# Optimization experiments

Hardware: AMD Instinct MI355X
Metric: run time of the kernel (lower is better)

## Reference

```python
import jax, jax.numpy as jnp
import numpy as np
from jax import lax

B, N, D, S, K = 8, 4096, 61, 1024, 32
MLP = (64, 64, 128)
WN = (3, 8, 8, 16)  # WeightNet: 3 -> 8 -> 8 -> 16
EPS = 1e-5


def _gather(p, idx):
    # p: [B, N, C], idx: [B, ...] -> [B, ..., C]
    return jax.vmap(lambda pb, ib: pb[ib])(p, idx)


def _fps(xyz, npoint, key):
    # farthest point sampling, xyz: [B, N, 3] -> idx [B, npoint]
    b, n, _ = xyz.shape
    start = jax.random.randint(key, (b,), 0, n)
    def step(carry, _):
        dmin, far = carry
        centroid = jnp.take_along_axis(xyz, far[:, None, None], axis=1)  # [B,1,3]
        d = jnp.sum((xyz - centroid) ** 2, -1)                            # [B,N]
        dmin = jnp.minimum(dmin, d)
        return (dmin, jnp.argmax(dmin, -1)), far
    _, idxs = lax.scan(step, (jnp.full((b, n), 1e10, xyz.dtype), start), None, length=npoint)
    return idxs.T  # [B, npoint]


def _sqdist(a, b):
    # a: [B,S,3], b: [B,N,3] -> [B,S,N]
    return (jnp.sum(a ** 2, -1)[:, :, None] + jnp.sum(b ** 2, -1)[:, None, :]
            - 2.0 * jnp.einsum('bsc,bnc->bsn', a, b))


def _bn_relu(x, g, be):
    # channels-last BN (training-mode batch stats, biased var) + ReLU
    axes = tuple(range(x.ndim - 1))
    m = x.mean(axes, keepdims=True)
    v = x.var(axes, keepdims=True)
    return jax.nn.relu(g * (x - m) * lax.rsqrt(v + EPS) + be)


def _forward(xyz, points, mlp_p, wn_p, lin_w, lin_b, bnl_g, bnl_b):
    xyz_t = xyz.transpose(0, 2, 1)    # [B,N,3]
    pts = points.transpose(0, 2, 1)   # [B,N,D]
    xyz_sg = lax.stop_gradient(xyz_t)  # index computations carry no grads (as in torch)
    fps_idx = _fps(xyz_sg, S, jax.random.key(42))  # [B,S]
    new_xyz = _gather(xyz_t, fps_idx)              # [B,S,3]
    idx = lax.top_k(-_sqdist(lax.stop_gradient(new_xyz), xyz_sg), K)[1]  # [B,S,K]
    g_norm = _gather(xyz_t, idx) - new_xyz[:, :, None, :]                # [B,S,K,3]
    feat = jnp.concatenate([g_norm, _gather(pts, idx)], -1)              # [B,S,K,3+D]
    for w, b, g, be in mlp_p:
        feat = _bn_relu(jnp.einsum('bskc,oc->bsko', feat, w) + b, g, be)
    wts = g_norm
    for w, b, g, be in wn_p:
        wts = _bn_relu(jnp.einsum('bskc,oc->bsko', wts, w) + b, g, be)   # [B,S,K,16]
    # [B,S,C,K] @ [B,S,K,16] -> [B,S,C,16] -> [B,S,C*16] (C-major flatten, as torch .view)
    agg = jnp.einsum('bskc,bskw->bscw', feat, wts).reshape(B, S, -1)
    out = agg @ lin_w.T + lin_b                                          # [B,S,128]
    m = out.mean((0, 1), keepdims=True)  # BatchNorm1d over batch and spatial
    v = out.var((0, 1), keepdims=True)
    out = jax.nn.relu(bnl_g * (out - m) * lax.rsqrt(v + EPS) + bnl_b)
    return new_xyz.transpose(0, 2, 1), out.transpose(0, 2, 1)  # [B,3,S], [B,128,S]


def setup_inputs() -> dict:
    key = jax.random.key(0)
    ks = iter(jax.random.split(key, 64))
    inp = {"xyz": jax.random.normal(next(ks), (B, 3, N), jnp.float32),
           "points": jax.random.normal(next(ks), (B, D, N), jnp.float32)}
    mlp_in = (3 + D,) + MLP[:-1]
    for i, (ci, co) in enumerate(zip(mlp_in, MLP)):
        inp[f"mlp_w{i}"] = jax.random.normal(next(ks), (co, ci), jnp.float32) / np.float32(np.sqrt(ci))
        inp[f"mlp_b{i}"] = jnp.zeros((co,), jnp.float32)
        inp[f"mlp_g{i}"] = jnp.ones((co,), jnp.float32)
        inp[f"mlp_be{i}"] = jnp.zeros((co,), jnp.float32)
    for i, (ci, co) in enumerate(zip(WN[:-1], WN[1:])):
        inp[f"wn_w{i}"] = jax.random.normal(next(ks), (co, ci), jnp.float32) / np.float32(np.sqrt(ci))
        inp[f"wn_b{i}"] = jnp.zeros((co,), jnp.float32)
        inp[f"wn_g{i}"] = jnp.ones((co,), jnp.float32)
        inp[f"wn_be{i}"] = jnp.zeros((co,), jnp.float32)
    fin = 16 * MLP[-1]
    inp["lin_w"] = jax.random.normal(next(ks), (MLP[-1], fin), jnp.float32) / np.float32(np.sqrt(fin))
    inp["lin_b"] = jnp.zeros((MLP[-1],), jnp.float32)
    inp["bnl_g"] = jnp.ones((MLP[-1],), jnp.float32)
    inp["bnl_b"] = jnp.zeros((MLP[-1],), jnp.float32)
    return inp


def reference(xyz, points, mlp_w0, mlp_b0, mlp_g0, mlp_be0, mlp_w1, mlp_b1, mlp_g1, mlp_be1, mlp_w2, mlp_b2, mlp_g2, mlp_be2, wn_w0, wn_b0, wn_g0, wn_be0, wn_w1, wn_b1, wn_g1, wn_be1, wn_w2, wn_b2, wn_g2, wn_be2, lin_w, lin_b, bnl_g, bnl_b):
    mlp_p = [(mlp_w0, mlp_b0, mlp_g0, mlp_be0),
             (mlp_w1, mlp_b1, mlp_g1, mlp_be1),
             (mlp_w2, mlp_b2, mlp_g2, mlp_be2)]
    wn_p = [(wn_w0, wn_b0, wn_g0, wn_be0),
            (wn_w1, wn_b1, wn_g1, wn_be1),
            (wn_w2, wn_b2, wn_g2, wn_be2)]
    return _forward(xyz, points, mlp_p, wn_p, lin_w, lin_b, bnl_g, bnl_b)
```

## Files before the change

kernel.cpp:

```cpp
#include <hip/hip_runtime.h>
#include <cstdint>
#include <cstddef>


constexpr int B_ = 8, N_ = 4096, D_ = 61, S_ = 1024, K_ = 32;
constexpr int P_ = B_ * S_ * K_;
constexpr int BS_ = B_ * S_;

constexpr size_t OFF_STATS  = 0;
constexpr size_t OFF_NEWXYZ = 8192;
constexpr size_t OFF_KNN    = 106496;
constexpr size_t OFF_PT     = 1155072;
constexpr size_t OFF_Y01    = 9543680;
constexpr size_t OFF_Y2     = 76652544;
constexpr size_t OFF_W01    = 210870272;
constexpr size_t OFF_W2B    = 219258880;
constexpr size_t OFF_OUTPRE = OFF_W01;

static inline uint32_t rotl32(uint32_t x, int r){ return (x << r) | (x >> (32 - r)); }
static void tf2x32(uint32_t k0, uint32_t k1, uint32_t x0, uint32_t x1,
                   uint32_t* o0, uint32_t* o1){
  uint32_t ks[3] = {k0, k1, k0 ^ k1 ^ 0x1BD11BDAu};
  x0 += ks[0]; x1 += ks[1];
  const int RA[4] = {13,15,26,6}, RB[4] = {17,29,16,24};
// ... 5 lines not shown
  *o0 = x0; *o1 = x1;
}
struct StartIdx { int v[8]; };
static StartIdx compute_starts(){
  uint32_t ka, kb;
  tf2x32(0u, 42u, 0u, 1u, &ka, &kb);
  StartIdx s;
  for (int i = 0; i < 8; ++i){
    uint32_t b1, b2;
    tf2x32(ka, kb, 0u, (uint32_t)i, &b1, &b2);
    s.v[i] = (int)((b1 ^ b2) & 4095u);
  }
  return s;
}

template<int C>
__device__ __forceinline__ float dpp_max_f32_step(float x){
  int t = __builtin_amdgcn_update_dpp(0, (int)__float_as_uint(x), C, 0xf, 0xf, true);
  return fmaxf(x, __uint_as_float((unsigned)t));
}
__device__ __forceinline__ float dpp_wave_max_f32(float x){
  x = dpp_max_f32_step<0x111>(x);
  x = dpp_max_f32_step<0x112>(x);
  x = dpp_max_f32_step<0x114>(x);
  x = dpp_max_f32_step<0x118>(x);
  x = dpp_max_f32_step<0x142>(x);
  x = dpp_max_f32_step<0x143>(x);
  return __uint_as_float((unsigned)__builtin_amdgcn_readlane((int)__float_as_uint(x), 63));
}
template<int C>
__device__ __forceinline__ unsigned dpp_min_u32_step(unsigned x){
  int t = __builtin_amdgcn_update_dpp(-1, (int)x, C, 0xf, 0xf, false);
  unsigned u = (unsigned)t;
  return u < x ? u : x;
}
__device__ __forceinline__ unsigned dpp_wave_min_u32(unsigned x){
  x = dpp_min_u32_step<0x111>(x);
  x = dpp_min_u32_step<0x112>(x);
  x = dpp_min_u32_step<0x114>(x);
  x = dpp_min_u32_step<0x118>(x);
  x = dpp_min_u32_step<0x142>(x);
  x = dpp_min_u32_step<0x143>(x);
  return (unsigned)__builtin_amdgcn_readlane((int)x, 63);
}
template<int C>
__device__ __forceinline__ unsigned long long dpp_min_u64_step(unsigned long long k){
  unsigned lo = (unsigned)k, hi = (unsigned)(k >> 32);
  unsigned olo = (unsigned)__builtin_amdgcn_update_dpp(-1, (int)lo, C, 0xf, 0xf, false);
  unsigned ohi = (unsigned)__builtin_amdgcn_update_dpp(-1, (int)hi, C, 0xf, 0xf, false);
  unsigned long long o = ((unsigned long long)ohi << 32) | olo;
  return o < k ? o : k;
}
__device__ __forceinline__ unsigned long long dpp_wave_min_u64(unsigned long long k){
  k = dpp_min_u64_step<0x111>(k);
  k = dpp_min_u64_step<0x112>(k);
  k = dpp_min_u64_step<0x114>(k);
  k = dpp_min_u64_step<0x118>(k);
  k = dpp_min_u64_step<0x142>(k);
  k = dpp_min_u64_step<0x143>(k);
  unsigned lo = (unsigned)__builtin_amdgcn_readlane((int)(unsigned)k, 63);
  unsigned hi = (unsigned)__builtin_amdgcn_readlane((int)(unsigned)(k >> 32), 63);
  return ((unsigned long long)hi << 32) | lo;
}
template<int C>
__device__ __forceinline__ float dpp_add_step(float x){
  int t = __builtin_amdgcn_update_dpp(0, (int)__float_as_uint(x), C, 0xf, 0xf, true);
  return x + __uint_as_float((unsigned)t);
}
__device__ __forceinline__ float dpp_row_sum16(float x){
  x = dpp_add_step<0x111>(x);
  x = dpp_add_step<0x112>(x);
  x = dpp_add_step<0x114>(x);
  x = dpp_add_step<0x118>(x);
  return x;
}
__device__ __forceinline__ unsigned ordf(float f){
  unsigned u = __float_as_uint(f);
  return u ^ (unsigned)(((int)u >> 31) | 0x80000000);
}
__device__ __forceinline__ void atomAddD(double* p, double v){
  __hip_atomic_fetch_add(p, v, __ATOMIC_RELAXED, __HIP_MEMORY_SCOPE_AGENT);
}

#define REP16(M) M(0) M(1) M(2) M(3) M(4) M(5) M(6) M(7) \
                 M(8) M(9) M(10) M(11) M(12) M(13) M(14) M(15)

__global__ __launch_bounds__(256, 1) void fps_tr_kernel(const float* __restrict__ xyz,
                                                        const float* __restrict__ pts,
                                                        StartIdx st,
                                                        float* __restrict__ new_xyz,
                                                        float* __restrict__ out_xyz,
                                                        float* __restrict__ pT){
  __shared__ float4 pts4[N_];
  __shared__ unsigned short win[S_];
  __shared__ unsigned long long slotK[2][4];
  __shared__ float4 slotC[2][4];
  const int tid = threadIdx.x;

  if (blockIdx.x >= 8){
    float* tile = (float*)pts4;
    const int tt = blockIdx.x - 8;
    const int b = tt >> 6, n0 = (tt & 63) * 64;
    for (int e = tid; e < 61*64; e += 256){
      int d = e >> 6, c = e & 63;
      tile[d*65 + c] = pts[((size_t)b*61 + d)*N_ + n0 + c];
    }
    __syncthreads();
    for (int e = tid; e < 4096; e += 256){
      int r = e >> 6, d = e & 63;
      pT[((size_t)b*N_ + n0 + r)*64 + d] = (d < 61) ? tile[d*65 + r] : 0.f;
    }
    return;
  }

  const int b = blockIdx.x;
  const int lane = tid & 63, wv = tid >> 6;
  const float* xb = xyz + (size_t)b*3*N_;

#define LOADP(i) \
  float px##i = xb[tid + 256*(i)]; \
  float py##i = xb[N_ + tid + 256*(i)]; \
  float pz##i = xb[2*N_ + tid + 256*(i)]; \
  float dm##i = 1e10f; \
  pts4[tid + 256*(i)] = make_float4(px##i, py##i, pz##i, 0.f);
  REP16(LOADP)
#undef LOADP
  __syncthreads();

  int cur = st.v[b];
  float4 c4 = pts4[cur];
  float cx = c4.x, cy = c4.y, cz = c4.z;

  int par = 0;
  for (int s = 0; s < S_; ++s){
    if (tid == 0) win[s] = (unsigned short)cur;
#define UPD(i) { \
      float dx = __fsub_rn(px##i, cx), dy = __fsub_rn(py##i, cy), dz = __fsub_rn(pz##i, cz); \
      float d  = __fadd_rn(__fadd_rn(__fmul_rn(dx,dx), __fmul_rn(dy,dy)), __fmul_rn(dz,dz)); \
      dm##i = fminf(dm##i, d); }
    REP16(UPD)
#undef UPD
    float a0 = fmaxf(dm0, dm1),  a1 = fmaxf(dm2, dm3);
    float a2 = fmaxf(dm4, dm5),  a3 = fmaxf(dm6, dm7);
    float a4 = fmaxf(dm8, dm9),  a5 = fmaxf(dm10, dm11);
    float a6 = fmaxf(dm12, dm13),a7 = fmaxf(dm14, dm15);
    float b0 = fmaxf(a0, a1), b1 = fmaxf(a2, a3), b2 = fmaxf(a4, a5), b3 = fmaxf(a6, a7);
    float lmax = fmaxf(fmaxf(b0, b1), fmaxf(b2, b3));
    const float wmax = dpp_wave_max_f32(lmax);
#define CANDI(i) unsigned c##i = (dm##i == wmax) ? (unsigned)(tid | ((i) << 8)) : 0xFFFFFFFFu;
    REP16(CANDI)
#undef CANDI
    unsigned d0 = c0  < c1  ? c0  : c1,  d1 = c2  < c3  ? c2  : c3;
    unsigned d2 = c4  < c5  ? c4  : c5,  d3 = c6  < c7  ? c6  : c7;
    unsigned d4 = c8  < c9  ? c8  : c9,  d5 = c10 < c11 ? c10 : c11;
    unsigned d6 = c12 < c13 ? c12 : c13, d7 = c14 < c15 ? c14 : c15;
    unsigned e0 = d0 < d1 ? d0 : d1, e1 = d2 < d3 ? d2 : d3;
    unsigned e2 = d4 < d5 ? d4 : d5, e3 = d6 < d7 ? d6 : d7;
    unsigned f0 = e0 < e1 ? e0 : e1, f1 = e2 < e3 ? e2 : e3;
    unsigned cand = f0 < f1 ? f0 : f1;
    const unsigned widx = dpp_wave_min_u32(cand);
    if (tid == (int)(widx & 255u)){
      const int sl = (int)(widx >> 8);
      float sx = px0, sy = py0, sz = pz0;
#define SEL(i) if (sl == (i)){ sx = px##i; sy = py##i; sz = pz##i; }
      SEL(1) SEL(2) SEL(3) SEL(4) SEL(5) SEL(6) SEL(7) SEL(8)
      SEL(9) SEL(10) SEL(11) SEL(12) SEL(13) SEL(14) SEL(15)
#undef SEL
      slotK[par][wv] = ((unsigned long long)__float_as_uint(wmax) << 32)
                     | (unsigned long long)(unsigned)(~widx);
      slotC[par][wv] = make_float4(sx, sy, sz, 0.f);
    }
    __syncthreads();
    unsigned long long k0 = slotK[par][0], k1 = slotK[par][1],
                       k2 = slotK[par][2], k3 = slotK[par][3];
    float4 q0 = slotC[par][0], q1 = slotC[par][1],
           q2 = slotC[par][2], q3 = slotC[par][3];
    unsigned long long m0 = k0; float4 g0 = q0;
    if (k1 > m0){ m0 = k1; g0 = q1; }
    unsigned long long m1 = k2; float4 g1 = q2;
    if (k3 > m1){ m1 = k3; g1 = q3; }
    if (m1 > m0){ m0 = m1; g0 = g1; }
    cur = (int)(~(unsigned)m0) & (N_ - 1);
    cx = g0.x; cy = g0.y; cz = g0.z;
    par ^= 1;
  }
  __syncthreads();
  for (int s2 = tid; s2 < S_; s2 += 256){
    float4 p = pts4[win[s2]];
    new_xyz[((size_t)b*S_ + s2)*3 + 0] = p.x;
    new_xyz[((size_t)b*S_ + s2)*3 + 1] = p.y;
    new_xyz[((size_t)b*S_ + s2)*3 + 2] = p.z;
    out_xyz[(size_t)b*3*S_ + s2]        = p.x;
    out_xyz[(size_t)b*3*S_ + S_ + s2]   = p.y;
    out_xyz[(size_t)b*3*S_ + 2*S_ + s2] = p.z;
  }
}
#undef REP16

__global__ __launch_bounds__(256) void knn_kernel(const float* __restrict__ xyz,
                                                  const float* __restrict__ nxyz,
                                                  int* __restrict__ knn_idx){
  __shared__ float dist[4][4096];
  const int wv = threadIdx.x >> 6, lane = threadIdx.x & 63;
  const int q = blockIdx.x*4 + wv;
  const int b = q >> 10;
  const float* xb = xyz + (size_t)b*3*N_;
  const float ax = nxyz[(size_t)q*3], ay = nxyz[(size_t)q*3+1], az = nxyz[(size_t)q*3+2];
  const float sa = __fadd_rn(__fadd_rn(__fmul_rn(ax,ax), __fmul_rn(ay,ay)), __fmul_rn(az,az));
  float* dw = dist[wv];
  unsigned long long kk = ~0ull;
  for (int i = 0; i < 64; ++i){
    int n = i*64 + lane;
    float x = xb[n], y = xb[N_+n], z = xb[2*N_+n];
    float sb  = __fadd_rn(__fadd_rn(__fmul_rn(x,x), __fmul_rn(y,y)), __fmul_rn(z,z));
    float dot = __fadd_rn(__fadd_rn(__fmul_rn(ax,x), __fmul_rn(ay,y)), __fmul_rn(az,z));
    float d   = __fsub_rn(__fadd_rn(sa, sb), __fmul_rn(2.f, dot));
    dw[i*64 + ((lane + i) & 63)] = d;
    unsigned long long key = ((unsigned long long)ordf(d) << 32) | (unsigned)n;
    if (key < kk) kk = key;
  }
  __syncthreads();
  int myout = 0;
  for (int r = 0; r < 32; ++r){
    unsigned long long g = dpp_wave_min_u64(kk);
    const int gn = (int)(g & 0xFFFFFFFFull);
    if (lane == r) myout = gn;
    const int col = gn & 63, row = gn >> 6;
    const int a = lane*64 + ((col + lane) & 63);
    float v = dw[a];
    if (lane == row){ v = 3.4e38f; dw[a] = 3.4e38f; }
    unsigned long long nk = ((unsigned long long)ordf(v) << 32)
                          | (unsigned)(lane*64 + col);
    nk = dpp_wave_min_u64(nk);
    if (lane == col) kk = nk;
  }
  if (lane < 32) knn_idx[(size_t)q*32 + lane] = myout;
}

__device__ __forceinline__ void bn_coeff(const double* st, const float* g, const float* be,
                                         int c, double cnt, float* sc, float* sh){
  double mean = st[c*2] / cnt;
  double var  = st[c*2+1] / cnt - mean*mean;
  double scale = (double)g[c] / sqrt(var + 1e-5);
  *sc = (float)scale; *sh = (float)((double)be[c] - mean*scale);
}

#define STATS64(ACC_EXPR, ST, CH_OFF)                                          \
  {                                                                            \
    _Pragma("unroll")                                                          \
    for (int o = 0; o < 64; ++o){                                              \
      float v_ = (ACC_EXPR);                                                   \
      float s1_ = dpp_row_sum16(v_);                                           \
      float q1_ = dpp_row_sum16(v_*v_);                                        \
      if ((threadIdx.x & 15) == 15){                                           \
        int rid_ = threadIdx.x >> 4;                                           \
        redS[rid_][o] = s1_; redQ[rid_][o] = q1_;                              \
      }                                                                        \
    }                                                                          \
    __syncthreads();                                                           \
    if (threadIdx.x < 64){                                                     \
      float s_ = 0.f;                                                          \
      _Pragma("unroll")                                                        \
      for (int r_ = 0; r_ < 16; ++r_) s_ += redS[r_][threadIdx.x];             \
      atomAddD(&(ST)[((CH_OFF) + threadIdx.x)*2], (double)s_);                 \
    } else if (threadIdx.x < 128){                                             \
      int o_ = threadIdx.x - 64;                                               \
      float s_ = 0.f;                                                          \
      _Pragma("unroll")                                                        \
      for (int r_ = 0; r_ < 16; ++r_) s_ += redQ[r_][o_];                      \
      atomAddD(&(ST)[((CH_OFF) + o_)*2 + 1], (double)s_);                      \
    }                                                                          \
  }

__global__ __launch_bounds__(256, 2) void m0_kernel(const float* __restrict__ pT,
                                                    const float* __restrict__ xyz,
                                                    const float* __restrict__ nxyz,
                                                    const int* __restrict__ knn_idx,
                                                    const float* __restrict__ w,
                                                    const float* __restrict__ bias,
                                                    float* __restrict__ y,
                                                    double* __restrict__ stout){
  __shared__ float Wt[4096]; __shared__ float bb[64];
  __shared__ float redS[16][65], redQ[16][65];
  for (int t = threadIdx.x; t < 4096; t += 256){ int o = t >> 6, c = t & 63; Wt[c*64+o] = w[o*64+c]; }
  if (threadIdx.x < 64) bb[threadIdx.x] = bias[threadIdx.x];
  __syncthreads();
  const int p = blockIdx.x*256 + threadIdx.x;
  const int b = p >> 15, s = (p & 32767) >> 5;
  const int n = knn_idx[p];
  float in[64];
  {
    const float* xb = xyz + (size_t)b*3*N_;
    const int q = (b << 10) + s;
    in[0] = xb[n]       - nxyz[(size_t)q*3];
    in[1] = xb[N_+n]    - nxyz[(size_t)q*3+1];
    in[2] = xb[2*N_+n]  - nxyz[(size_t)q*3+2];
    const float* pr = pT + ((size_t)b*N_ + n)*64;
#pragma unroll
    for (int d = 0; d < 60; d += 4){
      float4 v = *reinterpret_cast<const float4*>(&pr[d]);
      in[3+d] = v.x; in[4+d] = v.y; in[5+d] = v.z; in[6+d] = v.w;
    }
    in[63] = pr[60];
  }
  float acc[64];
#pragma unroll
  for (int o = 0; o < 64; ++o) acc[o] = bb[o];
#pragma unroll
  for (int c = 0; c < 64; ++c){
    float x = in[c];
#pragma unroll
    for (int o = 0; o < 64; o += 4){
      float4 w4 = *reinterpret_cast<const float4*>(&Wt[c*64+o]);
      acc[o]   += x*w4.x; acc[o+1] += x*w4.y; acc[o+2] += x*w4.z; acc[o+3] += x*w4.w;
    }
  }
#pragma unroll
  for (int o = 0; o < 64; ++o) y[(size_t)o*P_ + p] = acc[o];
  STATS64(acc[o], stout, 0)
}

__global__ __launch_bounds__(256, 2) void m1_kernel(float* __restrict__ y,
                                                    const float* __restrict__ w,
                                                    const float* __restrict__ bias,
                                                    const double* __restrict__ stin,
                                                    const float* __restrict__ g,
                                                    const float* __restrict__ be,
                                                    double* __restrict__ stout){
  __shared__ float Wt[4096]; __shared__ float bb[64], sc[64], sh[64];
  __shared__ float redS[16][65], redQ[16][65];
  for (int t = threadIdx.x; t < 4096; t += 256){ int o = t >> 6, c = t & 63; Wt[c*64+o] = w[o*64+c]; }
  if (threadIdx.x < 64){
    bn_coeff(stin, g, be, threadIdx.x, (double)P_, &sc[threadIdx.x], &sh[threadIdx.x]);
    bb[threadIdx.x] = bias[threadIdx.x];
  }
  __syncthreads();
  const int p = blockIdx.x*256 + threadIdx.x;
  float in[64];
#pragma unroll
  for (int c = 0; c < 64; ++c){
    float x = y[(size_t)c*P_ + p];
    in[c] = fmaxf(0.f, fmaf(x, sc[c], sh[c]));
  }
  float acc[64];
#pragma unroll
  for (int o = 0; o < 64; ++o) acc[o] = bb[o];
#pragma unroll
  for (int c = 0; c < 64; ++c){
    float x = in[c];
#pragma unroll
    for (int o = 0; o < 64; o += 4){
      float4 w4 = *reinterpret_cast<const float4*>(&Wt[c*64+o]);
      acc[o]   += x*w4.x; acc[o+1] += x*w4.y; acc[o+2] += x*w4.z; acc[o+3] += x*w4.w;
    }
  }
#pragma unroll
  for (int o = 0; o < 64; ++o) y[(size_t)o*P_ + p] = acc[o];
  STATS64(acc[o], stout, 0)
}

__global__ __launch_bounds__(256, 2) void m2_kernel(const float* __restrict__ y1,
                                                    float* __restrict__ y2,
                                                    const float* __restrict__ w,
                                                    const float* __restrict__ bias,
                                                    const double* __restrict__ stin,
                                                    const float* __restrict__ g,
                                                    const float* __restrict__ be,
                                                    double* __restrict__ stout){
  __shared__ float Wt[4096]; __shared__ float bb[64], sc[64], sh[64];
  __shared__ float redS[16][65], redQ[16][65];
  const int half = blockIdx.y;
  for (int t = threadIdx.x; t < 4096; t += 256){
    int o = t >> 6, c = t & 63;
    Wt[c*64+o] = w[(size_t)(half*64+o)*64 + c];
  }
  if (threadIdx.x < 64){
    bn_coeff(stin, g, be, threadIdx.x, (double)P_, &sc[threadIdx.x], &sh[threadIdx.x]);
    bb[threadIdx.x] = bias[half*64 + threadIdx.x];
  }
  __syncthreads();
  const int p = blockIdx.x*256 + threadIdx.x;
  float in[64];
#pragma unroll
  for (int c = 0; c < 64; ++c){
    float x = y1[(size_t)c*P_ + p];
    in[c] = fmaxf(0.f, fmaf(x, sc[c], sh[c]));
  }
  float acc[64];
#pragma unroll
  for (int o = 0; o < 64; ++o) acc[o] = bb[o];
#pragma unroll
  for (int c = 0; c < 64; ++c){
    float x = in[c];
#pragma unroll
    for (int o = 0; o < 64; o += 4){
      float4 w4 = *reinterpret_cast<const float4*>(&Wt[c*64+o]);
      acc[o]   += x*w4.x; acc[o+1] += x*w4.y; acc[o+2] += x*w4.z; acc[o+3] += x*w4.w;
    }
  }
#pragma unroll
  for (int o = 0; o < 64; ++o) y2[(size_t)(half*64+o)*P_ + p] = acc[o];
  STATS64(acc[o], stout, half*64)
}

__global__ __launch_bounds__(256) void w0_kernel(const float* __restrict__ xyz,
                                                 const float* __restrict__ nxyz,
                                                 const int* __restrict__ knn_idx,
                                                 const float* __restrict__ w,
                                                 const float* __restrict__ bias,
                                                 float* __restrict__ wb,
                                                 double* __restrict__ stout){
  __shared__ float Wl[24], bb[8];
  __shared__ float redS[16][9], redQ[16][9];
  if (threadIdx.x < 24) Wl[threadIdx.x] = w[threadIdx.x];
  if (threadIdx.x < 8)  bb[threadIdx.x] = bias[threadIdx.x];
  __syncthreads();
  const int p = blockIdx.x*256 + threadIdx.x;
  const int b = p >> 15, s = (p & 32767) >> 5;
  const int n = knn_idx[p];
  const float* xb = xyz + (size_t)b*3*N_;
  const int q = (b << 10) + s;
  float gx = xb[n]      - nxyz[(size_t)q*3];
  float gy = xb[N_+n]   - nxyz[(size_t)q*3+1];
  float gz = xb[2*N_+n] - nxyz[(size_t)q*3+2];
  float a_[8];
#pragma unroll
  for (int o = 0; o < 8; ++o){
    a_[o] = bb[o] + gx*Wl[o*3] + gy*Wl[o*3+1] + gz*Wl[o*3+2];
    wb[(size_t)o*P_ + p] = a_[o];
  }
#pragma unroll
  for (int o = 0; o < 8; ++o){
    float s1 = dpp_row_sum16(a_[o]);
    float q1 = dpp_row_sum16(a_[o]*a_[o]);
    if ((threadIdx.x & 15) == 15){ int rid = threadIdx.x >> 4; redS[rid][o] = s1; redQ[rid][o] = q1; }
  }
  __syncthreads();
  if (threadIdx.x < 8){
    float s_ = 0.f;
#pragma unroll
    for (int r = 0; r < 16; ++r) s_ += redS[r][threadIdx.x];
    atomAddD(&stout[threadIdx.x*2], (double)s_);
  } else if (threadIdx.x < 16){
    int o = threadIdx.x - 8;
    float s_ = 0.f;
#pragma unroll
    for (int r = 0; r < 16; ++r) s_ += redQ[r][o];
    atomAddD(&stout[o*2+1], (double)s_);
  }
}

__global__ __launch_bounds__(256) void w1_kernel(float* __restrict__ wb,
                                                 const float* __restrict__ w,
                                                 const float* __restrict__ bias,
                                                 const double* __restrict__ stin,
                                                 const float* __restrict__ g,
                                                 const float* __restrict__ be,
                                                 double* __restrict__ stout){
  __shared__ float Wl[64], bb[8], sc[8], sh[8];
  __shared__ float redS[16][9], redQ[16][9];
  if (threadIdx.x < 64) Wl[threadIdx.x] = w[threadIdx.x];
  if (threadIdx.x < 8){
    bn_coeff(stin, g, be, threadIdx.x, (double)P_, &sc[threadIdx.x], &sh[threadIdx.x]);
    bb[threadIdx.x] = bias[threadIdx.x];
  }
  __syncthreads();
  const int p = blockIdx.x*256 + threadIdx.x;
  float in[8];
#pragma unroll
  for (int c = 0; c < 8; ++c){
    float x = wb[(size_t)c*P_ + p];
    in[c] = fmaxf(0.f, fmaf(x, sc[c], sh[c]));
  }
  float acc[8];
#pragma unroll
  for (int o = 0; o < 8; ++o){
    float a = bb[o];
#pragma unroll
    for (int c = 0; c < 8; ++c) a += in[c]*Wl[o*8+c];
    acc[o] = a;
  }
#pragma unroll
  for (int o = 0; o < 8; ++o) wb[(size_t)o*P_ + p] = acc[o];
#pragma unroll
  for (int o = 0; o < 8; ++o){
    float s1 = dpp_row_sum16(acc[o]);
    float q1 = dpp_row_sum16(acc[o]*acc[o]);
    if ((threadIdx.x & 15) == 15){ int rid = threadIdx.x >> 4; redS[rid][o] = s1; redQ[rid][o] = q1; }
  }
  __syncthreads();
  if (threadIdx.x < 8){
    float s_ = 0.f;
#pragma unroll
    for (int r = 0; r < 16; ++r) s_ += redS[r][threadIdx.x];
    atomAddD(&stout[threadIdx.x*2], (double)s_);
  } else if (threadIdx.x < 16){
    int o = threadIdx.x - 8;
    float s_ = 0.f;
#pragma unroll
    for (int r = 0; r < 16; ++r) s_ += redQ[r][o];
    atomAddD(&stout[o*2+1], (double)s_);
  }
}

__global__ __launch_bounds__(256) void w2_kernel(const float* __restrict__ wb,
                                                 float* __restrict__ wb2,
                                                 const float* __restrict__ w,
                                                 const float* __restrict__ bias,
                                                 const double* __restrict__ stin,
                                                 const float* __restrict__ g,
                                                 const float* __restrict__ be,
                                                 double* __restrict__ stout){
  __shared__ float Wl[128], bb[16], sc[8], sh[8];
  __shared__ float redS[16][17], redQ[16][17];
  if (threadIdx.x < 128) Wl[threadIdx.x] = w[threadIdx.x];
  if (threadIdx.x < 8)
    bn_coeff(stin, g, be, threadIdx.x, (double)P_, &sc[threadIdx.x], &sh[threadIdx.x]);
  if (threadIdx.x < 16) bb[threadIdx.x] = bias[threadIdx.x];
  __syncthreads();
  const int p = blockIdx.x*256 + threadIdx.x;
  float in[8];
#pragma unroll
  for (int c = 0; c < 8; ++c){
    float x = wb[(size_t)c*P_ + p];
    in[c] = fmaxf(0.f, fmaf(x, sc[c], sh[c]));
  }
  float acc[16];
#pragma unroll
  for (int o = 0; o < 16; ++o){
    float a = bb[o];
#pragma unroll
    for (int c = 0; c < 8; ++c) a += in[c]*Wl[o*8+c];
    acc[o] = a;
    wb2[(size_t)o*P_ + p] = a;
  }
#pragma unroll
  for (int o = 0; o < 16; ++o){
    float s1 = dpp_row_sum16(acc[o]);
    float q1 = dpp_row_sum16(acc[o]*acc[o]);
    if ((threadIdx.x & 15) == 15){ int rid = threadIdx.x >> 4; redS[rid][o] = s1; redQ[rid][o] = q1; }
  }
  __syncthreads();
  if (threadIdx.x < 16){
    float s_ = 0.f;
#pragma unroll
    for (int r = 0; r < 16; ++r) s_ += redS[r][threadIdx.x];
    atomAddD(&stout[threadIdx.x*2], (double)s_);
  } else if (threadIdx.x < 32){
    int o = threadIdx.x - 16;
    float s_ = 0.f;
#pragma unroll
    for (int r = 0; r < 16; ++r) s_ += redQ[r][o];
    atomAddD(&stout[o*2+1], (double)s_);
  }
}

__global__ __launch_bounds__(256) void agg_kernel(const float* __restrict__ y2,
                                                  const float* __restrict__ wb2,
                                                  const double* __restrict__ st2,
                                                  const float* __restrict__ g2,
                                                  const float* __restrict__ be2,
                                                  const double* __restrict__ stw,
                                                  const float* __restrict__ gw,
                                                  const float* __restrict__ bew,
                                                  float* __restrict__ agg){
  __shared__ float f[32*132];
  __shared__ float wt[32*16];
  __shared__ float sc2[128], sh2[128], scw[16], shw[16];
  const int t = threadIdx.x;
  if (t < 128) bn_coeff(st2, g2, be2, t, (double)P_, &sc2[t], &sh2[t]);
  if (t < 16)  bn_coeff(stw, gw, bew, t, (double)P_, &scw[t], &shw[t]);
  __syncthreads();
  const int bs = blockIdx.x;
  const size_t p0 = (size_t)bs * 32;
  for (int e = t; e < 4096; e += 256){
    int c = e >> 5, k = e & 31;
    float x = y2[(size_t)c*P_ + p0 + k];
    f[k*132 + c] = fmaxf(0.f, fmaf(x, sc2[c], sh2[c]));
  }
  for (int e = t; e < 512; e += 256){
    int w = e >> 5, k = e & 31;
    float x = wb2[(size_t)w*P_ + p0 + k];
    wt[k*16 + w] = fmaxf(0.f, fmaf(x, scw[w], shw[w]));
  }
  __syncthreads();
  const int c = t >> 1, wp = (t & 1) * 8;
  float a0=0,a1=0,a2=0,a3=0,a4=0,a5=0,a6=0,a7=0;
#pragma unroll
  for (int k = 0; k < 32; ++k){
    float fv = f[k*132 + c];
    float4 u = *reinterpret_cast<const float4*>(&wt[k*16 + wp]);
    float4 v = *reinterpret_cast<const float4*>(&wt[k*16 + wp + 4]);
    a0 += fv*u.x; a1 += fv*u.y; a2 += fv*u.z; a3 += fv*u.w;
    a4 += fv*v.x; a5 += fv*v.y; a6 += fv*v.z; a7 += fv*v.w;
  }
  float* dst = agg + (size_t)bs*2048 + c*16 + wp;
  *reinterpret_cast<float4*>(dst)     = make_float4(a0,a1,a2,a3);
  *reinterpret_cast<float4*>(dst + 4) = make_float4(a4,a5,a6,a7);
}

__global__ __launch_bounds__(256) void lin_kernel(const float* __restrict__ agg,
                                                  const float* __restrict__ lw,
                                                  const float* __restrict__ lb,
                                                  float* __restrict__ outp){
  __shared__ float A[32*33];
  __shared__ float Wl[32*128];
  __shared__ float lbs[128];
  const int t = threadIdx.x;
  const int r0 = blockIdx.x * 32;
  if (t < 128) lbs[t] = lb[t];
  const int c_lane = t & 31, rg = t >> 5;
  float acc[4][4];
#pragma unroll
  for (int i = 0; i < 4; ++i)
#pragma unroll
    for (int j = 0; j < 4; ++j) acc[i][j] = 0.f;

  for (int kk0 = 0; kk0 < 2048; kk0 += 32){
    __syncthreads();
    {
      int r = t >> 3, kq = (t & 7) * 4;
      float4 v = *reinterpret_cast<const float4*>(&agg[(size_t)(r0 + r)*2048 + kk0 + kq]);
      A[r*33 + kq]   = v.x; A[r*33 + kq+1] = v.y; A[r*33 + kq+2] = v.z; A[r*33 + kq+3] = v.w;
    }
    {
#pragma unroll
      for (int u = 0; u < 4; ++u){
        int fid = t + 256*u;
        int o = fid >> 3, kq = (fid & 7) * 4;
        float4 v = *reinterpret_cast<const float4*>(&lw[(size_t)o*2048 + kk0 + kq]);
        Wl[(kq  )*128 + o] = v.x; Wl[(kq+1)*128 + o] = v.y;
        Wl[(kq+2)*128 + o] = v.z; Wl[(kq+3)*128 + o] = v.w;
      }
    }
    __syncthreads();
#pragma unroll 8
// ... 19 lines not shown

__global__ __launch_bounds__(128) void statsF_kernel(const float* __restrict__ outp,
                                                     double* __restrict__ st){
  const int c = threadIdx.x;
  const int r0 = blockIdx.x * 128;
  double s = 0.0, q = 0.0;
  for (int r = 0; r < 128; ++r){
    double v = outp[(size_t)(r0 + r)*128 + c];
    s += v; q += v*v;
  }
  atomAddD(&st[c*2], s); atomAddD(&st[c*2+1], q);
}

__global__ __launch_bounds__(256) void final_kernel(const float* __restrict__ outp,
                                                    const double* __restrict__ st,
                                                    const float* __restrict__ g,
                                                    const float* __restrict__ be,
                                                    float* __restrict__ out){
  __shared__ float sc[128], sh[128];
  __shared__ float tile[64][129];
  const int t = threadIdx.x;
  if (t < 128) bn_coeff(st, g, be, t, (double)BS_, &sc[t], &sh[t]);
  const int bs0 = blockIdx.x * 64;
  const int b = bs0 >> 10, s0 = bs0 & 1023;
#pragma unroll
  for (int e = t; e < 8192; e += 256){
    int r = e >> 7, c = e & 127;
    tile[r][c] = outp[(size_t)(bs0 + r)*128 + c];
  }
  __syncthreads();
#pragma unroll
  for (int e = t; e < 8192; e += 256){
    int o = e >> 6, si = e & 63;
    float x = tile[si][o];
    out[(size_t)b*131072 + (size_t)o*1024 + s0 + si] = fmaxf(0.f, fmaf(x, sc[o], sh[o]));
  }
}

extern "C" void kernel_launch(void* const* d_in, const int* in_sizes, int n_in,
                              void* d_out, int out_size, void* d_ws, size_t ws_size,
                              hipStream_t stream){
  (void)in_sizes; (void)n_in; (void)out_size; (void)ws_size;
  const float* xyz    = (const float*)d_in[0];
  const float* points = (const float*)d_in[1];
  const float* mw0 = (const float*)d_in[2],  *mb0 = (const float*)d_in[3],
             * mg0 = (const float*)d_in[4],  *me0 = (const float*)d_in[5];
  const float* mw1 = (const float*)d_in[6],  *mb1 = (const float*)d_in[7],
             * mg1 = (const float*)d_in[8],  *me1 = (const float*)d_in[9];
  const float* mw2 = (const float*)d_in[10], *mb2 = (const float*)d_in[11],
             * mg2 = (const float*)d_in[12], *me2 = (const float*)d_in[13];
  const float* ww0 = (const float*)d_in[14], *wb0 = (const float*)d_in[15],
             * wg0 = (const float*)d_in[16], *we0 = (const float*)d_in[17];
  const float* ww1 = (const float*)d_in[18], *wb1 = (const float*)d_in[19],
             * wg1 = (const float*)d_in[20], *we1 = (const float*)d_in[21];
  const float* ww2 = (const float*)d_in[22], *wb2_ = (const float*)d_in[23],
             * wg2 = (const float*)d_in[24], *we2 = (const float*)d_in[25];
  const float* lw  = (const float*)d_in[26], *lb  = (const float*)d_in[27];
  const float* fg  = (const float*)d_in[28], *fb  = (const float*)d_in[29];

  char* ws = (char*)d_ws;
  double* ST0 = (double*)(ws + OFF_STATS);
  double* ST1 = (double*)(ws + OFF_STATS + 1024);
  double* ST2 = (double*)(ws + OFF_STATS + 2048);
  double* SW0 = (double*)(ws + OFF_STATS + 4096);
  double* SW1 = (double*)(ws + OFF_STATS + 4224);
  double* SW2 = (double*)(ws + OFF_STATS + 4352);
  double* STF = (double*)(ws + OFF_STATS + 4608);
  float* nxyz   = (float*)(ws + OFF_NEWXYZ);
  int*   knnidx = (int*)(ws + OFF_KNN);
  float* pT     = (float*)(ws + OFF_PT);
  float* y01    = (float*)(ws + OFF_Y01);
  float* y2     = (float*)(ws + OFF_Y2);
  float* w01    = (float*)(ws + OFF_W01);
  float* w2b    = (float*)(ws + OFF_W2B);
  float* aggbuf = (float*)(ws + OFF_Y01);
  float* outpre = (float*)(ws + OFF_OUTPRE);

  float* out_xyz  = (float*)d_out;
  float* out_feat = (float*)d_out + (size_t)B_*3*S_;

  hipMemsetAsync(ws + OFF_STATS, 0, 8192, stream);

  StartIdx st = compute_starts();
  fps_tr_kernel<<<dim3(8 + B_*64), dim3(256), 0, stream>>>(xyz, points, st, nxyz, out_xyz, pT);

  knn_kernel<<<dim3(BS_/4), dim3(256), 0, stream>>>(xyz, nxyz, knnidx);

  m0_kernel<<<dim3(P_/256), dim3(256), 0, stream>>>(pT, xyz, nxyz, knnidx, mw0, mb0, y01, ST0);
  m1_kernel<<<dim3(P_/256), dim3(256), 0, stream>>>(y01, mw1, mb1, ST0, mg0, me0, ST1);
  m2_kernel<<<dim3(P_/256, 2), dim3(256), 0, stream>>>(y01, y2, mw2, mb2, ST1, mg1, me1, ST2);

  w0_kernel<<<dim3(P_/256), dim3(256), 0, stream>>>(xyz, nxyz, knnidx, ww0, wb0, w01, SW0);
  w1_kernel<<<dim3(P_/256), dim3(256), 0, stream>>>(w01, ww1, wb1, SW0, wg0, we0, SW1);
  w2_kernel<<<dim3(P_/256), dim3(256), 0, stream>>>(w01, w2b, ww2, wb2_, SW1, wg1, we1, SW2);

  agg_kernel<<<dim3(BS_), dim3(256), 0, stream>>>(y2, w2b, ST2, mg2, me2, SW2, wg2, we2, aggbuf);
  lin_kernel<<<dim3(BS_/32), dim3(256), 0, stream>>>(aggbuf, lw, lb, outpre);
  statsF_kernel<<<dim3(BS_/128), dim3(128), 0, stream>>>(outpre, STF);
  final_kernel<<<dim3(BS_/64), dim3(256), 0, stream>>>(outpre, STF, fg, fb, out_feat);
}
```

Measured before the change: 1.772 ms.

## Fuse WeightNet layers into MLP kernels and widen FPS block to 512 threads

The three WeightNet kernels (w0/w1/w2) are folded into the corresponding MLP layer kernels, so the gathered xyz offsets and per-point work share one launch and one index gather. This removes three launches and the separate xyz re-gather. FPS now runs with 512 threads per batch, 8 points per thread instead of 16, and a cross-wave reduction over 8 waves. It also skips the unused distance update on the final iteration. The trade-off is more registers and shared memory in the fused MLP kernels, and an extra wave in the per-iteration FPS barrier reduction.

```diff
diff --git a/kernel.cpp b/kernel.cpp
--- a/kernel.cpp
+++ b/kernel.cpp
@@ -111,10 +111,9 @@
   __hip_atomic_fetch_add(p, v, __ATOMIC_RELAXED, __HIP_MEMORY_SCOPE_AGENT);
 }
 
-#define REP16(M) M(0) M(1) M(2) M(3) M(4) M(5) M(6) M(7) \
-                 M(8) M(9) M(10) M(11) M(12) M(13) M(14) M(15)
-
-__global__ __launch_bounds__(256, 1) void fps_tr_kernel(const float* __restrict__ xyz,
+#define REP8(M) M(0) M(1) M(2) M(3) M(4) M(5) M(6) M(7)
+
+__global__ __launch_bounds__(512, 1) void fps_tr_kernel(const float* __restrict__ xyz,
                                                         const float* __restrict__ pts,
                                                         StartIdx st,
                                                         float* __restrict__ new_xyz,
@@ -122,20 +121,20 @@
                                                         float* __restrict__ pT){
   __shared__ float4 pts4[N_];
   __shared__ unsigned short win[S_];
-  __shared__ unsigned long long slotK[2][4];
-  __shared__ float4 slotC[2][4];
+  __shared__ unsigned long long slotK[2][8];
+  __shared__ float4 slotC[2][8];
   const int tid = threadIdx.x;
 
   if (blockIdx.x >= 8){
     float* tile = (float*)pts4;
     const int tt = blockIdx.x - 8;
     const int b = tt >> 6, n0 = (tt & 63) * 64;
-    for (int e = tid; e < 61*64; e += 256){
+    for (int e = tid; e < 61*64; e += 512){
       int d = e >> 6, c = e & 63;
       tile[d*65 + c] = pts[((size_t)b*61 + d)*N_ + n0 + c];
     }
     __syncthreads();
-    for (int e = tid; e < 4096; e += 256){
+    for (int e = tid; e < 4096; e += 512){
       int r = e >> 6, d = e & 63;
       pT[((size_t)b*N_ + n0 + r)*64 + d] = (d < 61) ? tile[d*65 + r] : 0.f;
     }
@@ -147,12 +146,12 @@
   const float* xb = xyz + (size_t)b*3*N_;
 
 #define LOADP(i) \
-  float px##i = xb[tid + 256*(i)]; \
-  float py##i = xb[N_ + tid + 256*(i)]; \
-  float pz##i = xb[2*N_ + tid + 256*(i)]; \
+  float px##i = xb[tid + 512*(i)]; \
+  float py##i = xb[N_ + tid + 512*(i)]; \
+  float pz##i = xb[2*N_ + tid + 512*(i)]; \
   float dm##i = 1e10f; \
-  pts4[tid + 256*(i)] = make_float4(px##i, py##i, pz##i, 0.f);
-  REP16(LOADP)
+  pts4[tid + 512*(i)] = make_float4(px##i, py##i, pz##i, 0.f);
+  REP8(LOADP)
 #undef LOADP
   __syncthreads();
 
@@ -163,37 +162,30 @@
   int par = 0;
   for (int s = 0; s < S_; ++s){
     if (tid == 0) win[s] = (unsigned short)cur;
+    if (s == S_ - 1) break;
 #define UPD(i) { \
       float dx = __fsub_rn(px##i, cx), dy = __fsub_rn(py##i, cy), dz = __fsub_rn(pz##i, cz); \
       float d  = __fadd_rn(__fadd_rn(__fmul_rn(dx,dx), __fmul_rn(dy,dy)), __fmul_rn(dz,dz)); \
       dm##i = fminf(dm##i, d); }
-    REP16(UPD)
+    REP8(UPD)
 #undef UPD
-    float a0 = fmaxf(dm0, dm1),  a1 = fmaxf(dm2, dm3);
-    float a2 = fmaxf(dm4, dm5),  a3 = fmaxf(dm6, dm7);
-    float a4 = fmaxf(dm8, dm9),  a5 = fmaxf(dm10, dm11);
-    float a6 = fmaxf(dm12, dm13),a7 = fmaxf(dm14, dm15);
-    float b0 = fmaxf(a0, a1), b1 = fmaxf(a2, a3), b2 = fmaxf(a4, a5), b3 = fmaxf(a6, a7);
-    float lmax = fmaxf(fmaxf(b0, b1), fmaxf(b2, b3));
+    float a0 = fmaxf(dm0, dm1), a1 = fmaxf(dm2, dm3);
+    float a2 = fmaxf(dm4, dm5), a3 = fmaxf(dm6, dm7);
+    float lmax = fmaxf(fmaxf(a0, a1), fmaxf(a2, a3));
     const float wmax = dpp_wave_max_f32(lmax);
-#define CANDI(i) unsigned c##i = (dm##i == wmax) ? (unsigned)(tid | ((i) << 8)) : 0xFFFFFFFFu;
-    REP16(CANDI)
+#define CANDI(i) unsigned c##i = (dm##i == wmax) ? (unsigned)(tid | ((i) << 9)) : 0xFFFFFFFFu;
+    REP8(CANDI)
 #undef CANDI
-    unsigned d0 = c0  < c1  ? c0  : c1,  d1 = c2  < c3  ? c2  : c3;
-    unsigned d2 = c4  < c5  ? c4  : c5,  d3 = c6  < c7  ? c6  : c7;
-    unsigned d4 = c8  < c9  ? c8  : c9,  d5 = c10 < c11 ? c10 : c11;
-    unsigned d6 = c12 < c13 ? c12 : c13, d7 = c14 < c15 ? c14 : c15;
+    unsigned d0 = c0 < c1 ? c0 : c1, d1 = c2 < c3 ? c2 : c3;
+    unsigned d2 = c4 < c5 ? c4 : c5, d3 = c6 < c7 ? c6 : c7;
     unsigned e0 = d0 < d1 ? d0 : d1, e1 = d2 < d3 ? d2 : d3;
-    unsigned e2 = d4 < d5 ? d4 : d5, e3 = d6 < d7 ? d6 : d7;
-    unsigned f0 = e0 < e1 ? e0 : e1, f1 = e2 < e3 ? e2 : e3;
-    unsigned cand = f0 < f1 ? f0 : f1;
+    unsigned cand = e0 < e1 ? e0 : e1;
     const unsigned widx = dpp_wave_min_u32(cand);
-    if (tid == (int)(widx & 255u)){
-      const int sl = (int)(widx >> 8);
+    if (tid == (int)(widx & 511u)){
+      const int sl = (int)(widx >> 9);
       float sx = px0, sy = py0, sz = pz0;
 #define SEL(i) if (sl == (i)){ sx = px##i; sy = py##i; sz = pz##i; }
-      SEL(1) SEL(2) SEL(3) SEL(4) SEL(5) SEL(6) SEL(7) SEL(8)
-      SEL(9) SEL(10) SEL(11) SEL(12) SEL(13) SEL(14) SEL(15)
+      SEL(1) SEL(2) SEL(3) SEL(4) SEL(5) SEL(6) SEL(7)
 #undef SEL
       slotK[par][wv] = ((unsigned long long)__float_as_uint(wmax) << 32)
                      | (unsigned long long)(unsigned)(~widx);
@@ -201,20 +193,26 @@
     }
     __syncthreads();
     unsigned long long k0 = slotK[par][0], k1 = slotK[par][1],
-                       k2 = slotK[par][2], k3 = slotK[par][3];
+                       k2 = slotK[par][2], k3 = slotK[par][3],
+                       k4 = slotK[par][4], k5 = slotK[par][5],
+                       k6 = slotK[par][6], k7 = slotK[par][7];
     float4 q0 = slotC[par][0], q1 = slotC[par][1],
-           q2 = slotC[par][2], q3 = slotC[par][3];
-    unsigned long long m0 = k0; float4 g0 = q0;
-    if (k1 > m0){ m0 = k1; g0 = q1; }
-    unsigned long long m1 = k2; float4 g1 = q2;
-    if (k3 > m1){ m1 = k3; g1 = q3; }
+           q2 = slotC[par][2], q3 = slotC[par][3],
+           q4 = slotC[par][4], q5 = slotC[par][5],
+           q6 = slotC[par][6], q7 = slotC[par][7];
+    unsigned long long m0 = k0; float4 g0 = q0; if (k1 > m0){ m0 = k1; g0 = q1; }
+    unsigned long long m1 = k2; float4 g1 = q2; if (k3 > m1){ m1 = k3; g1 = q3; }
+    unsigned long long m2 = k4; float4 g2 = q4; if (k5 > m2){ m2 = k5; g2 = q5; }
+    unsigned long long m3 = k6; float4 g3 = q6; if (k7 > m3){ m3 = k7; g3 = q7; }
     if (m1 > m0){ m0 = m1; g0 = g1; }
+    if (m3 > m2){ m2 = m3; g2 = g3; }
+    if (m2 > m0){ m0 = m2; g0 = g2; }
     cur = (int)(~(unsigned)m0) & (N_ - 1);
     cx = g0.x; cy = g0.y; cz = g0.z;
     par ^= 1;
   }
   __syncthreads();
-  for (int s2 = tid; s2 < S_; s2 += 256){
+  for (int s2 = tid; s2 < S_; s2 += 512){
     float4 p = pts4[win[s2]];
     new_xyz[((size_t)b*S_ + s2)*3 + 0] = p.x;
     new_xyz[((size_t)b*S_ + s2)*3 + 1] = p.y;
@@ -224,7 +222,7 @@
     out_xyz[(size_t)b*3*S_ + 2*S_ + s2] = p.z;
   }
 }
-#undef REP16
+#undef REP8
 
 __global__ __launch_bounds__(256) void knn_kernel(const float* __restrict__ xyz,
                                                   const float* __restrict__ nxyz,
@@ -301,18 +299,52 @@
     }                                                                          \
   }
 
-__global__ __launch_bounds__(256, 2) void m0_kernel(const float* __restrict__ pT,
-                                                    const float* __restrict__ xyz,
-                                                    const float* __restrict__ nxyz,
-                                                    const int* __restrict__ knn_idx,
-                                                    const float* __restrict__ w,
-                                                    const float* __restrict__ bias,
-                                                    float* __restrict__ y,
-                                                    double* __restrict__ stout){
+#define STATSW(NC, VALS, ST)                                                   \
+  {                                                                            \
+    _Pragma("unroll")                                                          \
+    for (int o = 0; o < (NC); ++o){                                            \
+      float s1 = dpp_row_sum16(VALS[o]);                                       \
+      float q1 = dpp_row_sum16(VALS[o]*VALS[o]);                               \
+      if ((threadIdx.x & 15) == 15){                                           \
+        int rid = threadIdx.x >> 4;                                            \
+        redSW[rid][o] = s1; redQW[rid][o] = q1;                                \
+      }                                                                        \
+    }                                                                          \
+    __syncthreads();                                                           \
+    if (threadIdx.x < (NC)){                                                   \
+      float s_ = 0.f;                                                          \
+      _Pragma("unroll")                                                        \
+      for (int r = 0; r < 16; ++r) s_ += redSW[r][threadIdx.x];                \
+      atomAddD(&(ST)[threadIdx.x*2], (double)s_);                              \
+    } else if (threadIdx.x < 2*(NC)){                                          \
+      int o = threadIdx.x - (NC);                                              \
+      float s_ = 0.f;                                                          \
+      _Pragma("unroll")                                                        \
+      for (int r = 0; r < 16; ++r) s_ += redQW[r][o];                          \
+      atomAddD(&(ST)[o*2+1], (double)s_);                                      \
+    }                                                                          \
+  }
+
+__global__ __launch_bounds__(256, 2) void m0w0_kernel(const float* __restrict__ pT,
+                                                      const float* __restrict__ xyz,
+                                                      const float* __restrict__ nxyz,
+                                                      const int* __restrict__ knn_idx,
+                                                      const float* __restrict__ w,
+                                                      const float* __restrict__ bias,
+                                                      const float* __restrict__ ww0,
+                                                      const float* __restrict__ wb0,
+                                                      float* __restrict__ y,
+                                                      float* __restrict__ wbuf,
+                                                      double* __restrict__ stout,
+                                                      double* __restrict__ stw){
   __shared__ float Wt[4096]; __shared__ float bb[64];
+  __shared__ float Wl0[24], bb0[8];
   __shared__ float redS[16][65], redQ[16][65];
+  __shared__ float redSW[16][9], redQW[16][9];
   for (int t = threadIdx.x; t < 4096; t += 256){ int o = t >> 6, c = t & 63; Wt[c*64+o] = w[o*64+c]; }
   if (threadIdx.x < 64) bb[threadIdx.x] = bias[threadIdx.x];
+  if (threadIdx.x >= 64 && threadIdx.x < 88) Wl0[threadIdx.x-64] = ww0[threadIdx.x-64];
+  if (threadIdx.x >= 96 && threadIdx.x < 104) bb0[threadIdx.x-96] = wb0[threadIdx.x-96];
   __syncthreads();
   const int p = blockIdx.x*256 + threadIdx.x;
   const int b = p >> 15, s = (p & 32767) >> 5;
@@ -332,6 +364,12 @@
     }
     in[63] = pr[60];
   }
+  float wa[8];
+#pragma unroll
+  for (int o = 0; o < 8; ++o){
+    wa[o] = bb0[o] + in[0]*Wl0[o*3] + in[1]*Wl0[o*3+1] + in[2]*Wl0[o*3+2];
+    wbuf[(size_t)o*P_ + p] = wa[o];
+  }
   float acc[64];
 #pragma unroll
   for (int o = 0; o < 64; ++o) acc[o] = bb[o];
@@ -347,24 +385,57 @@
 #pragma unroll
   for (int o = 0; o < 64; ++o) y[(size_t)o*P_ + p] = acc[o];
   STATS64(acc[o], stout, 0)
-}
-
-__global__ __launch_bounds__(256, 2) void m1_kernel(float* __restrict__ y,
-                                                    const float* __restrict__ w,
-                                                    const float* __restrict__ bias,
-                                                    const double* __restrict__ stin,
-                                                    const float* __restrict__ g,
-                                                    const float* __restrict__ be,
-                                                    double* __restrict__ stout){
+  __syncthreads();
+  STATSW(8, wa, stw)
+}
+
+__global__ __launch_bounds__(256, 2) void m1w1_kernel(float* __restrict__ y,
+                                                      const float* __restrict__ w,
+                                                      const float* __restrict__ bias,
+                                                      const double* __restrict__ stin,
+                                                      const float* __restrict__ g,
+                                                      const float* __restrict__ be,
+                                                      float* __restrict__ wbuf,
+                                                      const float* __restrict__ ww1,
+                                                      const float* __restrict__ wb1,
+                                                      const double* __restrict__ stwin,
+                                                      const float* __restrict__ wg,
+                                                      const float* __restrict__ we,
+                                                      double* __restrict__ stout,
+                                                      double* __restrict__ stw){
   __shared__ float Wt[4096]; __shared__ float bb[64], sc[64], sh[64];
+  __shared__ float Wl[64], bbw[8], scw[8], shw[8];
   __shared__ float redS[16][65], redQ[16][65];
+  __shared__ float redSW[16][9], redQW[16][9];
   for (int t = threadIdx.x; t < 4096; t += 256){ int o = t >> 6, c = t & 63; Wt[c*64+o] = w[o*64+c]; }
   if (threadIdx.x < 64){
     bn_coeff(stin, g, be, threadIdx.x, (double)P_, &sc[threadIdx.x], &sh[threadIdx.x]);
     bb[threadIdx.x] = bias[threadIdx.x];
+  } else if (threadIdx.x < 128){
+    Wl[threadIdx.x-64] = ww1[threadIdx.x-64];
+  } else if (threadIdx.x < 136){
+    int o = threadIdx.x - 128;
+    bn_coeff(stwin, wg, we, o, (double)P_, &scw[o], &shw[o]);
+    bbw[o] = wb1[o];
   }
   __syncthreads();
   const int p = blockIdx.x*256 + threadIdx.x;
+  float win8[8];
+#pragma unroll
+  for (int c = 0; c < 8; ++c){
+    float x = wbuf[(size_t)c*P_ + p];
+    win8[c] = fmaxf(0.f, fmaf(x, scw[c], shw[c]));
+  }
+  float wacc[8];
+#pragma unroll
+  for (int o = 0; o < 8; ++o){
+    float a = bbw[o];
+#pragma unroll
+    for (int c = 0; c < 8; ++c) a += win8[c]*Wl[o*8+c];
+    wacc[o] = a;
+  }
+#pragma unroll
+  for (int o = 0; o < 8; ++o) wbuf[(size_t)o*P_ + p] = wacc[o];
   float in[64];
 #pragma unroll
   for (int c = 0; c < 64; ++c){
@@ -386,18 +457,30 @@
 #pragma unroll
   for (int o = 0; o < 64; ++o) y[(size_t)o*P_ + p] = acc[o];
   STATS64(acc[o], stout, 0)
-}
-
-__global__ __launch_bounds__(256, 2) void m2_kernel(const float* __restrict__ y1,
-                                                    float* __restrict__ y2,
-                                                    const float* __restrict__ w,
-                                                    const float* __restrict__ bias,
-                                                    const double* __restrict__ stin,
-                                                    const float* __restrict__ g,
-                                                    const float* __restrict__ be,
-                                                    double* __restrict__ stout){
+  __syncthreads();
+  STATSW(8, wacc, stw)
+}
+
+__global__ __launch_bounds__(256, 2) void m2w2_kernel(const float* __restrict__ y1,
+                                                      float* __restrict__ y2,
+                                                      const float* __restrict__ w,
+                                                      const float* __restrict__ bias,
+                                                      const double* __restrict__ stin,
+                                                      const float* __restrict__ g,
+                                                      const float* __restrict__ be,
+                                                      const float* __restrict__ wbuf,
+                                                      float* __restrict__ wbuf2,
+                                                      const float* __restrict__ ww2,
+                                                      const float* __restrict__ wb2,
+                                                      const double* __restrict__ stwin,
+                                                      const float* __restrict__ wg,
+                                                      const float* __restrict__ we,
+                                                      double* __restrict__ stout,
+                                                      double* __restrict__ stw){
   __shared__ float Wt[4096]; __shared__ float bb[64], sc[64], sh[64];
+  __shared__ float Wl[128], bbw[16], scw[8], shw[8];
   __shared__ float redS[16][65], redQ[16][65];
+  __shared__ float redSW[16][17], redQW[16][17];
   const int half = blockIdx.y;
   for (int t = threadIdx.x; t < 4096; t += 256){
     int o = t >> 6, c = t & 63;
@@ -406,9 +489,33 @@
   if (threadIdx.x < 64){
     bn_coeff(stin, g, be, threadIdx.x, (double)P_, &sc[threadIdx.x], &sh[threadIdx.x]);
     bb[threadIdx.x] = bias[half*64 + threadIdx.x];
+  } else if (threadIdx.x < 192){
+    Wl[threadIdx.x-64] = ww2[threadIdx.x-64];
+  } else if (threadIdx.x < 200){
+    int o = threadIdx.x - 192;
+    bn_coeff(stwin, wg, we, o, (double)P_, &scw[o], &shw[o]);
+  } else if (threadIdx.x < 216){
+    bbw[threadIdx.x-200] = wb2[threadIdx.x-200];
   }
   __syncthreads();
   const int p = blockIdx.x*256 + threadIdx.x;
+  float wacc[16];
+  if (half == 0){
+    float win8[8];
+#pragma unroll
+    for (int c = 0; c < 8; ++c){
+      float x = wbuf[(size_t)c*P_ + p];
+      win8[c] = fmaxf(0.f, fmaf(x, scw[c], shw[c]));
+    }
+#pragma unroll
+    for (int o = 0; o < 16; ++o){
+      float a = bbw[o];
+#pragma unroll
+      for (int c = 0; c < 8; ++c) a += win8[c]*Wl[o*8+c];
+      wacc[o] = a;
+      wbuf2[(size_t)o*P_ + p] = a;
+    }
+  }
   float in[64];
 #pragma unroll
   for (int c = 0; c < 64; ++c){
@@ -430,157 +537,9 @@
 #pragma unroll
   for (int o = 0; o < 64; ++o) y2[(size_t)(half*64+o)*P_ + p] = acc[o];
   STATS64(acc[o], stout, half*64)
-}
-
-__global__ __launch_bounds__(256) void w0_kernel(const float* __restrict__ xyz,
-                                                 const float* __restrict__ nxyz,
-                                                 const int* __restrict__ knn_idx,
-                                                 const float* __restrict__ w,
-                                                 const float* __restrict__ bias,
-                                                 float* __restrict__ wb,
-                                                 double* __restrict__ stout){
-  __shared__ float Wl[24], bb[8];
-  __shared__ float redS[16][9], redQ[16][9];
-  if (threadIdx.x < 24) Wl[threadIdx.x] = w[threadIdx.x];
-  if (threadIdx.x < 8)  bb[threadIdx.x] = bias[threadIdx.x];
-  __syncthreads();
-  const int p = blockIdx.x*256 + threadIdx.x;
-  const int b = p >> 15, s = (p & 32767) >> 5;
-  const int n = knn_idx[p];
-  const float* xb = xyz + (size_t)b*3*N_;
-  const int q = (b << 10) + s;
-  float gx = xb[n]      - nxyz[(size_t)q*3];
-  float gy = xb[N_+n]   - nxyz[(size_t)q*3+1];
-  float gz = xb[2*N_+n] - nxyz[(size_t)q*3+2];
-  float a_[8];
-#pragma unroll
-  for (int o = 0; o < 8; ++o){
-    a_[o] = bb[o] + gx*Wl[o*3] + gy*Wl[o*3+1] + gz*Wl[o*3+2];
-    wb[(size_t)o*P_ + p] = a_[o];
-  }
-#pragma unroll
-  for (int o = 0; o < 8; ++o){
-    float s1 = dpp_row_sum16(a_[o]);
-    float q1 = dpp_row_sum16(a_[o]*a_[o]);
-    if ((threadIdx.x & 15) == 15){ int rid = threadIdx.x >> 4; redS[rid][o] = s1; redQ[rid][o] = q1; }
-  }
-  __syncthreads();
-  if (threadIdx.x < 8){
-    float s_ = 0.f;
-#pragma unroll
-    for (int r = 0; r < 16; ++r) s_ += redS[r][threadIdx.x];
-    atomAddD(&stout[threadIdx.x*2], (double)s_);
-  } else if (threadIdx.x < 16){
-    int o = threadIdx.x - 8;
-    float s_ = 0.f;
-#pragma unroll
-    for (int r = 0; r < 16; ++r) s_ += redQ[r][o];
-    atomAddD(&stout[o*2+1], (double)s_);
-  }
-}
-
-__global__ __launch_bounds__(256) void w1_kernel(float* __restrict__ wb,
-                                                 const float* __restrict__ w,
-                                                 const float* __restrict__ bias,
-                                                 const double* __restrict__ stin,
-                                                 const float* __restrict__ g,
-                                                 const float* __restrict__ be,
-                                                 double* __restrict__ stout){
-  __shared__ float Wl[64], bb[8], sc[8], sh[8];
-  __shared__ float redS[16][9], redQ[16][9];
-  if (threadIdx.x < 64) Wl[threadIdx.x] = w[threadIdx.x];
-  if (threadIdx.x < 8){
-    bn_coeff(stin, g, be, threadIdx.x, (double)P_, &sc[threadIdx.x], &sh[threadIdx.x]);
-    bb[threadIdx.x] = bias[threadIdx.x];
-  }
-  __syncthreads();
-  const int p = blockIdx.x*256 + threadIdx.x;
-  float in[8];
-#pragma unroll
-  for (int c = 0; c < 8; ++c){
-    float x = wb[(size_t)c*P_ + p];
-    in[c] = fmaxf(0.f, fmaf(x, sc[c], sh[c]));
-  }
-  float acc[8];
-#pragma unroll
-  for (int o = 0; o < 8; ++o){
-    float a = bb[o];
-#pragma unroll
-    for (int c = 0; c < 8; ++c) a += in[c]*Wl[o*8+c];
-    acc[o] = a;
-  }
-#pragma unroll
-  for (int o = 0; o < 8; ++o) wb[(size_t)o*P_ + p] = acc[o];
-#pragma unroll
-  for (int o = 0; o < 8; ++o){
-    float s1 = dpp_row_sum16(acc[o]);
-    float q1 = dpp_row_sum16(acc[o]*acc[o]);
-    if ((threadIdx.x & 15) == 15){ int rid = threadIdx.x >> 4; redS[rid][o] = s1; redQ[rid][o] = q1; }
-  }
-  __syncthreads();
-  if (threadIdx.x < 8){
-    float s_ = 0.f;
-#pragma unroll
-    for (int r = 0; r < 16; ++r) s_ += redS[r][threadIdx.x];
-    atomAddD(&stout[threadIdx.x*2], (double)s_);
-  } else if (threadIdx.x < 16){
-    int o = threadIdx.x - 8;
-    float s_ = 0.f;
-#pragma unroll
-    for (int r = 0; r < 16; ++r) s_ += redQ[r][o];
-    atomAddD(&stout[o*2+1], (double)s_);
-  }
-}
-
-__global__ __launch_bounds__(256) void w2_kernel(const float* __restrict__ wb,
-                                                 float* __restrict__ wb2,
-                                                 const float* __restrict__ w,
-                                                 const float* __restrict__ bias,
-                                                 const double* __restrict__ stin,
-                                                 const float* __restrict__ g,
-                                                 const float* __restrict__ be,
-                                                 double* __restrict__ stout){
-  __shared__ float Wl[128], bb[16], sc[8], sh[8];
-  __shared__ float redS[16][17], redQ[16][17];
-  if (threadIdx.x < 128) Wl[threadIdx.x] = w[threadIdx.x];
-  if (threadIdx.x < 8)
-    bn_coeff(stin, g, be, threadIdx.x, (double)P_, &sc[threadIdx.x], &sh[threadIdx.x]);
-  if (threadIdx.x < 16) bb[threadIdx.x] = bias[threadIdx.x];
-  __syncthreads();
-  const int p = blockIdx.x*256 + threadIdx.x;
-  float in[8];
-#pragma unroll
-  for (int c = 0; c < 8; ++c){
-    float x = wb[(size_t)c*P_ + p];
-    in[c] = fmaxf(0.f, fmaf(x, sc[c], sh[c]));
-  }
-  float acc[16];
-#pragma unroll
-  for (int o = 0; o < 16; ++o){
-    float a = bb[o];
-#pragma unroll
-    for (int c = 0; c < 8; ++c) a += in[c]*Wl[o*8+c];
-    acc[o] = a;
-    wb2[(size_t)o*P_ + p] = a;
-  }
-#pragma unroll
-  for (int o = 0; o < 16; ++o){
-    float s1 = dpp_row_sum16(acc[o]);
-    float q1 = dpp_row_sum16(acc[o]*acc[o]);
-    if ((threadIdx.x & 15) == 15){ int rid = threadIdx.x >> 4; redS[rid][o] = s1; redQ[rid][o] = q1; }
-  }
-  __syncthreads();
-  if (threadIdx.x < 16){
-    float s_ = 0.f;
-#pragma unroll
-    for (int r = 0; r < 16; ++r) s_ += redS[r][threadIdx.x];
-    atomAddD(&stout[threadIdx.x*2], (double)s_);
-  } else if (threadIdx.x < 32){
-    int o = threadIdx.x - 16;
-    float s_ = 0.f;
-#pragma unroll
-    for (int r = 0; r < 16; ++r) s_ += redQ[r][o];
-    atomAddD(&stout[o*2+1], (double)s_);
+  if (half == 0){
+    __syncthreads();
+    STATSW(16, wacc, stw)
   }
 }
 
@@ -766,17 +725,19 @@
   hipMemsetAsync(ws + OFF_STATS, 0, 8192, stream);
 
   StartIdx st = compute_starts();
-  fps_tr_kernel<<<dim3(8 + B_*64), dim3(256), 0, stream>>>(xyz, points, st, nxyz, out_xyz, pT);
+  fps_tr_kernel<<<dim3(8 + B_*64), dim3(512), 0, stream>>>(xyz, points, st, nxyz, out_xyz, pT);
 
   knn_kernel<<<dim3(BS_/4), dim3(256), 0, stream>>>(xyz, nxyz, knnidx);
 
-  m0_kernel<<<dim3(P_/256), dim3(256), 0, stream>>>(pT, xyz, nxyz, knnidx, mw0, mb0, y01, ST0);
-  m1_kernel<<<dim3(P_/256), dim3(256), 0, stream>>>(y01, mw1, mb1, ST0, mg0, me0, ST1);
-  m2_kernel<<<dim3(P_/256, 2), dim3(256), 0, stream>>>(y01, y2, mw2, mb2, ST1, mg1, me1, ST2);
-
-  w0_kernel<<<dim3(P_/256), dim3(256), 0, stream>>>(xyz, nxyz, knnidx, ww0, wb0, w01, SW0);
-  w1_kernel<<<dim3(P_/256), dim3(256), 0, stream>>>(w01, ww1, wb1, SW0, wg0, we0, SW1);
-  w2_kernel<<<dim3(P_/256), dim3(256), 0, stream>>>(w01, w2b, ww2, wb2_, SW1, wg1, we1, SW2);
+  m0w0_kernel<<<dim3(P_/256), dim3(256), 0, stream>>>(pT, xyz, nxyz, knnidx,
+                                                      mw0, mb0, ww0, wb0,
+                                                      y01, w01, ST0, SW0);
+  m1w1_kernel<<<dim3(P_/256), dim3(256), 0, stream>>>(y01, mw1, mb1, ST0, mg0, me0,
+                                                      w01, ww1, wb1, SW0, wg0, we0,
+                                                      ST1, SW1);
+  m2w2_kernel<<<dim3(P_/256, 2), dim3(256), 0, stream>>>(y01, y2, mw2, mb2, ST1, mg1, me1,
+                                                         w01, w2b, ww2, wb2_, SW1, wg1, we1,
+                                                         ST2, SW2);
 
   agg_kernel<<<dim3(BS_), dim3(256), 0, stream>>>(y2, w2b, ST2, mg2, me2, SW2, wg2, we2, aggbuf);
   lin_kernel<<<dim3(BS_/32), dim3(256), 0, stream>>>(aggbuf, lw, lb, outpre);
```

After: 1.999 ms. +12.8%, slower.
